# Kernel tuning notes

Hardware: AMD Instinct MI355X
Metric: run time of the kernel (lower is better)

Reference implementation:

```python
import jax, jax.numpy as jnp
import numpy as np
from jax import lax

CIN, COUT, K_EXP, KSZ = 128, 256, 8, 3
HIDDEN = CIN // 4  # reduction=4
B, H, W = 32, 56, 56
TEMP = 1.0


def setup_inputs() -> dict:
    key = jax.random.key(0)
    ks = jax.random.split(key, 6)
    x = jax.random.normal(ks[0], (B, CIN, H, W), dtype=jnp.float32)
    weight_bank = jax.random.normal(ks[1], (K_EXP, COUT, CIN, KSZ, KSZ), dtype=jnp.float32) * 0.02
    fc1_w = jax.random.normal(ks[2], (HIDDEN, CIN), dtype=jnp.float32) * (1.0 / np.sqrt(CIN))
    fc1_b = jnp.zeros((HIDDEN,), dtype=jnp.float32)
    fc2_w = jax.random.normal(ks[3], (K_EXP, HIDDEN), dtype=jnp.float32) * (1.0 / np.sqrt(HIDDEN))
    fc2_b = jnp.zeros((K_EXP,), dtype=jnp.float32)
    return {"x": x, "weight_bank": weight_bank, "fc1_w": fc1_w, "fc1_b": fc1_b,
            "fc2_w": fc2_w, "fc2_b": fc2_b}


def reference(x, weight_bank, fc1_w, fc1_b, fc2_w, fc2_b):
    b, cin, h, w = x.shape
    # Routing: GAP -> fc1 -> relu -> fc2 -> softmax(/T)
    v = jnp.mean(x, axis=(2, 3))                       # (B, cin)
    hdd = jax.nn.relu(v @ fc1_w.T + fc1_b)             # (B, hidden)
    logits = hdd @ fc2_w.T + fc2_b                     # (B, K)
    a = jax.nn.softmax(logits / TEMP, axis=1)          # (B, K)
    # Per-sample dynamic weights: (B, cout, cin, k, k)
    Wdyn = jnp.einsum('bk,kocij->bocij', a, weight_bank)
    # Batched per-sample conv via grouped convolution:
    # x -> (1, B*cin, H, W), Wdyn -> (B*cout, cin, k, k), groups=B
    xg = x.reshape(1, b * cin, h, w)
    wg = Wdyn.reshape(b * weight_bank.shape[1], cin, KSZ, KSZ)
    y = lax.conv_general_dilated(
        xg, wg,
        window_strides=(1, 1),
        padding=[(1, 1), (1, 1)],
        feature_group_count=b,
        dimension_numbers=('NCHW', 'OIHW', 'NCHW'),
    )
    return y.reshape(b, weight_bank.shape[1], y.shape[2], y.shape[3])
```

## Files before the change

kernel.cpp:

```cpp
#include <hip/hip_runtime.h>


#define CIN    128
#define COUT   256
#define KEXP   8
#define HIDDEN 32
#define B_     32
#define H_     56
#define W_     56
#define HW     3136
#define HP     58
#define WP     66
#define KK     1152

typedef float  v4f  __attribute__((ext_vector_type(4)));
typedef __bf16 v8bf __attribute__((ext_vector_type(8)));

__device__ __forceinline__ unsigned short f2bf(float x) {
  unsigned int u = __float_as_uint(x);
  u += 0x7fff + ((u >> 16) & 1);
  return (unsigned short)(u >> 16);
}
__device__ __forceinline__ float bf2f(unsigned short s) {
  return __uint_as_float(((unsigned int)s) << 16);
}

__device__ __forceinline__ void gl_lds16(const void* g, void* lds) {
  __builtin_amdgcn_global_load_lds(
      (__attribute__((address_space(1))) void*)(unsigned long long)(g),
      (__attribute__((address_space(3))) void*)(lds),
      16, 0, 0);
}

__global__ __launch_bounds__(256) void k_xpose(const float* __restrict__ x,
                                               unsigned short* __restrict__ xpt,
                                               float* __restrict__ v) {
  const int h = blockIdx.x, b = blockIdx.y, tid = threadIdx.x;
  __shared__ float tf[56 * 129];
  __shared__ float gp[256];
  const float4* xr4 = (const float4*)x + (size_t)b * CIN * 784;

#pragma unroll
  for (int it = 0; it < 7; ++it) {
    int idx = it * 256 + tid;
    int c  = idx / 14;
    int wq = idx - c * 14;
    float4 q = xr4[(size_t)c * 784 + h * 14 + wq];
    int w0 = wq * 4;
    tf[(w0 + 0) * 129 + c] = q.x;
    tf[(w0 + 1) * 129 + c] = q.y;
    tf[(w0 + 2) * 129 + c] = q.z;
    tf[(w0 + 3) * 129 + c] = q.w;
  }
  __syncthreads();

  {
    int c = tid & 127, half = tid >> 7;
    float s = 0.f;
#pragma unroll
    for (int w = half * 28; w < half * 28 + 28; ++w) s += tf[w * 129 + c];
    gp[tid] = s;
  }

#pragma unroll
  for (int it = 0; it < 7; ++it) {
    int idx = it * 256 + tid;
    int w  = idx >> 5;
    int c4 = (idx & 31) << 2;
    ushort4 o;
    o.x = f2bf(tf[w * 129 + c4 + 0]);
    o.y = f2bf(tf[w * 129 + c4 + 1]);
    o.z = f2bf(tf[w * 129 + c4 + 2]);
    o.w = f2bf(tf[w * 129 + c4 + 3]);
    *(ushort4*)(xpt + ((size_t)(b * HP + (h + 1)) * WP + (w + 1)) * CIN + c4) = o;
  }
  __syncthreads();
  if (tid < 128)
    atomicAdd(v + b * CIN + tid, (gp[tid] + gp[tid + 128]) * (1.0f / 3136.0f));
}

__global__ void k_mlp(const float* __restrict__ v, const float* __restrict__ fc1w,
                      const float* __restrict__ fc1b, const float* __restrict__ fc2w,
                      const float* __restrict__ fc2b, float* __restrict__ aout) {
  const int b = blockIdx.x, t = threadIdx.x;
  __shared__ float hid[HIDDEN];
  __shared__ float lg[KEXP];
  if (t < HIDDEN) {
    float s = fc1b[t];
    const float* vb = v + b * CIN;
    const float* wr = fc1w + t * CIN;
    for (int c = 0; c < CIN; ++c) s += vb[c] * wr[c];
    hid[t] = fmaxf(s, 0.f);
  }
  __syncthreads();
  if (t < KEXP) {
    float s = fc2b[t];
    const float* wr = fc2w + t * HIDDEN;
    for (int j = 0; j < HIDDEN; ++j) s += hid[j] * wr[j];
    lg[t] = s;
  }
  __syncthreads();
  if (t == 0) {
    float m = lg[0];
    for (int k = 1; k < KEXP; ++k) m = fmaxf(m, lg[k]);
    float e[KEXP], den = 0.f;
    for (int k = 0; k < KEXP; ++k) { e[k] = expf(lg[k] - m); den += e[k]; }
    float inv = 1.0f / den;
    for (int k = 0; k < KEXP; ++k) aout[b * KEXP + k] = e[k] * inv;
  }
}

__global__ __launch_bounds__(256) void k_wdyn(const float* __restrict__ aout,
                                              const float* __restrict__ bank,
                                              unsigned short* __restrict__ wdyn) {
  const int cout = blockIdx.x, tid = threadIdx.x;
  __shared__ float4 bS4[KEXP * 288];
  __shared__ float aS[B_ * KEXP];

#pragma unroll
  for (int k = 0; k < KEXP; ++k) {
    const float4* bp = (const float4*)(bank + (size_t)(k * COUT + cout) * KK);
    for (int it = tid; it < 288; it += 256) bS4[k * 288 + it] = bp[it];
  }
  aS[tid] = aout[tid];
  __syncthreads();

  const float* bS = (const float*)bS4;
  const int lane_kk = tid & 63;
  const int bg = tid >> 6;
  float areg[8][KEXP];
#pragma unroll
  for (int bi = 0; bi < 8; ++bi)
#pragma unroll
    for (int k = 0; k < KEXP; ++k) areg[bi][k] = aS[(bg * 8 + bi) * KEXP + k];

  for (int it = 0; it < 18; ++it) {
    int kk  = it * 64 + lane_kk;
    int khw = kk >> 7, cin = kk & 127;
    int e   = cin * 9 + khw;
    float vv[KEXP];
#pragma unroll
    for (int k = 0; k < KEXP; ++k) vv[k] = bS[k * KK + e];
#pragma unroll
    for (int bi = 0; bi < 8; ++bi) {
      float s = 0.f;
#pragma unroll
      for (int k = 0; k < KEXP; ++k) s += areg[bi][k] * vv[k];
      wdyn[(size_t)((bg * 8 + bi) * COUT + cout) * KK + kk] = f2bf(s);
    }
  }
}

__global__ __launch_bounds__(256) void k_conv(const unsigned short* __restrict__ wdyn,
                                              const unsigned short* __restrict__ xpt,
                                              float* __restrict__ out) {
  const int bx = blockIdx.x;
  const int b  = blockIdx.y;
  const int bm = bx & 1, rp = bx >> 1;
  const int h0 = rp * 2;
  const int tid = threadIdx.x;
  const int wv = tid >> 6, l = tid & 63;
  const int q = l >> 4, l15 = l & 15;
  const int mq = (wv & 1) * 64, nq = (wv >> 1) * 64;

  __shared__ __align__(16) unsigned short Ash[128 * 64];
  __shared__ __align__(16) unsigned short Bsh[128 * 64];

  const unsigned short* wb = wdyn + (size_t)(b * COUT + bm * 128) * KK;
  const unsigned short* xb = xpt + (size_t)b * HP * WP * CIN;

  v4f acc[4][4];
#pragma unroll
  for (int i = 0; i < 4; ++i)
#pragma unroll
    for (int j = 0; j < 4; ++j)
#pragma unroll
      for (int rr = 0; rr < 4; ++rr) acc[i][j][rr] = 0.f;

  for (int t = 0; t < 18; ++t) {
    const int khw = t >> 1, cinb = (t & 1) << 6;
    const int kh = khw / 3, kw = khw - 3 * kh;
#pragma unroll
    for (int it = 0; it < 4; ++it) {
      int g = it * 256 + tid;
      int row = g >> 3;
      int c = (g & 7) ^ (row & 7);
      gl_lds16(wb + (size_t)row * KK + t * 64 + c * 8,
               Ash + (it * 256 + wv * 64) * 8);
    }
#pragma unroll
    for (int it = 0; it < 4; ++it) {
      int g = it * 256 + tid;
      int p = g >> 3;
      int c = (g & 7) ^ (p & 7);
      int hh = h0 + (p >> 6) + kh;
      int ww = (p & 63) + kw;
      gl_lds16(xb + (size_t)(hh * WP + ww) * CIN + cinb + c * 8,
               Bsh + (it * 256 + wv * 64) * 8);
    }
    __syncthreads();
#pragma unroll
    for (int ks = 0; ks < 2; ++ks) {
      v8bf af[4], bfr[4];
#pragma unroll
      for (int i = 0; i < 4; ++i) {
        int row = mq + 16 * i + l15;
        int phys = (q + 4 * ks) ^ (row & 7);
        af[i] = *(const v8bf*)(Ash + (row * 8 + phys) * 8);
      }
#pragma unroll
      for (int j = 0; j < 4; ++j) {
        int p = nq + 16 * j + l15;
        int phys = (q + 4 * ks) ^ (p & 7);
        bfr[j] = *(const v8bf*)(Bsh + (p * 8 + phys) * 8);
      }
#pragma unroll
      for (int i = 0; i < 4; ++i)
#pragma unroll
        for (int j = 0; j < 4; ++j)
          acc[i][j] = __builtin_amdgcn_mfma_f32_16x16x32_bf16(af[i], bfr[j],
                                                              acc[i][j], 0, 0, 0);
    }
    __syncthreads();
  }

#pragma unroll
  for (int j = 0; j < 4; ++j) {
    int p = nq + 16 * j + l15;
    int w = p & 63, hr = h0 + (p >> 6);
    if (w < 56) {
#pragma unroll
      for (int i = 0; i < 4; ++i) {
        int cout = bm * 128 + mq + 16 * i + 4 * q;
        float* op = out + ((size_t)(b * COUT + cout) * H_ + hr) * W_ + w;
#pragma unroll
        for (int rr = 0; rr < 4; ++rr) op[(size_t)rr * HW] = acc[i][j][rr];
      }
    }
  }
}

extern "C" void kernel_launch(void* const* d_in, const int* in_sizes, int n_in,
                              void* d_out, int out_size, void* d_ws, size_t ws_size,
                              hipStream_t stream) {
  const float* x    = (const float*)d_in[0];
  const float* bank = (const float*)d_in[1];
  const float* fc1w = (const float*)d_in[2];
  const float* fc1b = (const float*)d_in[3];
  const float* fc2w = (const float*)d_in[4];
  const float* fc2b = (const float*)d_in[5];
  float* out = (float*)d_out;

  char* ws = (char*)d_ws;
  float* v    = (float*)(ws + 0);
  float* aout = (float*)(ws + 16384);
  unsigned short* wdyn = (unsigned short*)(ws + 17408);
  unsigned short* xpt  = (unsigned short*)(ws + 17408 + 18874368);

  hipMemsetAsync(v, 0, 16384, stream);
  hipMemsetAsync(xpt, 0, (size_t)B_ * HP * WP * CIN * 2, stream);

  k_xpose<<<dim3(H_, B_), 256, 0, stream>>>(x, xpt, v);
  k_mlp<<<dim3(B_), 64, 0, stream>>>(v, fc1w, fc1b, fc2w, fc2b, aout);
  k_wdyn<<<dim3(COUT), 256, 0, stream>>>(aout, bank, wdyn);
  k_conv<<<dim3(56, B_), 256, 0, stream>>>(wdyn, xpt, out);
}
```

Measured before the change: 264.1 us.

## Flatten conv pixel tiling, drop padded columns and memsets, deterministic GAP

The conv kernel now tiles over flattened 128-pixel chunks (50 tiles per image instead of 56 row-pair tiles padded to 64 columns), so no MMA work is spent on the 8 padding columns of each row. The padded input width shrinks from 66 to 58, and the halo is zeroed inside the transpose kernel, which removes the two memsets. GAP partials are written per row and summed in the MLP kernel instead of accumulated with atomics. The weight-mixing kernel moves to 512 threads with 4 samples per thread, and the last chunk clamps pixel indices, which adds some redundant loads.

Measured after the change: 250.0 us. 5.3% less time.

```diff
diff --git a/kernel.cpp b/kernel.cpp
--- a/kernel.cpp
+++ b/kernel.cpp
@@ -10,7 +10,7 @@
 #define W_     56
 #define HW     3136
 #define HP     58
-#define WP     66
+#define WP     58
 #define KK     1152
 
 typedef float  v4f  __attribute__((ext_vector_type(4)));
@@ -20,9 +20,6 @@
   unsigned int u = __float_as_uint(x);
   u += 0x7fff + ((u >> 16) & 1);
   return (unsigned short)(u >> 16);
-}
-__device__ __forceinline__ float bf2f(unsigned short s) {
-  return __uint_as_float(((unsigned int)s) << 16);
 }
 
 __device__ __forceinline__ void gl_lds16(const void* g, void* lds) {
@@ -34,7 +31,7 @@
 
 __global__ __launch_bounds__(256) void k_xpose(const float* __restrict__ x,
                                                unsigned short* __restrict__ xpt,
-                                               float* __restrict__ v) {
+                                               float* __restrict__ gpart) {
   const int h = blockIdx.x, b = blockIdx.y, tid = threadIdx.x;
   __shared__ float tf[56 * 129];
   __shared__ float gp[256];
@@ -74,22 +71,43 @@
     o.w = f2bf(tf[w * 129 + c4 + 3]);
     *(ushort4*)(xpt + ((size_t)(b * HP + (h + 1)) * WP + (w + 1)) * CIN + c4) = o;
   }
+
+  if (tid < 128) {
+    size_t rb = (size_t)(b * HP + (h + 1)) * WP * CIN;
+    xpt[rb + tid] = 0;
+    xpt[rb + 57 * CIN + tid] = 0;
+  }
+  if (h == 0 || h == 55) {
+    int hr = (h == 0) ? 0 : 57;
+    size_t rb = (size_t)(b * HP + hr) * WP * CIN;
+    ushort4 z; z.x = z.y = z.z = z.w = 0;
+    for (int i = tid; i < 1856; i += 256)
+      *(ushort4*)(xpt + rb + i * 4) = z;
+  }
+
   __syncthreads();
   if (tid < 128)
-    atomicAdd(v + b * CIN + tid, (gp[tid] + gp[tid + 128]) * (1.0f / 3136.0f));
-}
-
-__global__ void k_mlp(const float* __restrict__ v, const float* __restrict__ fc1w,
+    gpart[((size_t)h * B_ + b) * CIN + tid] =
+        (gp[tid] + gp[tid + 128]) * (1.0f / 3136.0f);
+}
+
+__global__ void k_mlp(const float* __restrict__ gpart, const float* __restrict__ fc1w,
                       const float* __restrict__ fc1b, const float* __restrict__ fc2w,
                       const float* __restrict__ fc2b, float* __restrict__ aout) {
   const int b = blockIdx.x, t = threadIdx.x;
+  __shared__ float vS[CIN];
   __shared__ float hid[HIDDEN];
   __shared__ float lg[KEXP];
+  {
+    float s = 0.f;
+    for (int h = 0; h < H_; ++h) s += gpart[((size_t)h * B_ + b) * CIN + t];
+    vS[t] = s;
+  }
+  __syncthreads();
   if (t < HIDDEN) {
     float s = fc1b[t];
-    const float* vb = v + b * CIN;
     const float* wr = fc1w + t * CIN;
-    for (int c = 0; c < CIN; ++c) s += vb[c] * wr[c];
+    for (int c = 0; c < CIN; ++c) s += vS[c] * wr[c];
     hid[t] = fmaxf(s, 0.f);
   }
   __syncthreads();
@@ -110,29 +128,28 @@
   }
 }
 
-__global__ __launch_bounds__(256) void k_wdyn(const float* __restrict__ aout,
+__global__ __launch_bounds__(512) void k_wdyn(const float* __restrict__ aout,
                                               const float* __restrict__ bank,
                                               unsigned short* __restrict__ wdyn) {
   const int cout = blockIdx.x, tid = threadIdx.x;
   __shared__ float4 bS4[KEXP * 288];
   __shared__ float aS[B_ * KEXP];
 
-#pragma unroll
-  for (int k = 0; k < KEXP; ++k) {
-    const float4* bp = (const float4*)(bank + (size_t)(k * COUT + cout) * KK);
-    for (int it = tid; it < 288; it += 256) bS4[k * 288 + it] = bp[it];
-  }
-  aS[tid] = aout[tid];
+  for (int idx = tid; idx < KEXP * 288; idx += 512) {
+    int k = idx / 288, r = idx - k * 288;
+    bS4[idx] = ((const float4*)(bank + (size_t)(k * COUT + cout) * KK))[r];
+  }
+  if (tid < 256) aS[tid] = aout[tid];
   __syncthreads();
 
   const float* bS = (const float*)bS4;
   const int lane_kk = tid & 63;
-  const int bg = tid >> 6;
-  float areg[8][KEXP];
-#pragma unroll
-  for (int bi = 0; bi < 8; ++bi)
-#pragma unroll
-    for (int k = 0; k < KEXP; ++k) areg[bi][k] = aS[(bg * 8 + bi) * KEXP + k];
+  const int sg = tid >> 6;
+  float areg[4][KEXP];
+#pragma unroll
+  for (int bi = 0; bi < 4; ++bi)
+#pragma unroll
+    for (int k = 0; k < KEXP; ++k) areg[bi][k] = aS[(sg * 4 + bi) * KEXP + k];
 
   for (int it = 0; it < 18; ++it) {
     int kk  = it * 64 + lane_kk;
@@ -142,11 +159,11 @@
 #pragma unroll
     for (int k = 0; k < KEXP; ++k) vv[k] = bS[k * KK + e];
 #pragma unroll
-    for (int bi = 0; bi < 8; ++bi) {
+    for (int bi = 0; bi < 4; ++bi) {
       float s = 0.f;
 #pragma unroll
       for (int k = 0; k < KEXP; ++k) s += areg[bi][k] * vv[k];
-      wdyn[(size_t)((bg * 8 + bi) * COUT + cout) * KK + kk] = f2bf(s);
+      wdyn[(size_t)((sg * 4 + bi) * COUT + cout) * KK + kk] = f2bf(s);
     }
   }
 }
@@ -156,8 +173,8 @@
                                               float* __restrict__ out) {
   const int bx = blockIdx.x;
   const int b  = blockIdx.y;
-  const int bm = bx & 1, rp = bx >> 1;
-  const int h0 = rp * 2;
+  const int bm = bx & 1, ch = bx >> 1;
+  const int p0 = ch * 128;
   const int tid = threadIdx.x;
   const int wv = tid >> 6, l = tid & 63;
   const int q = l >> 4, l15 = l & 15;
@@ -191,11 +208,13 @@
 #pragma unroll
     for (int it = 0; it < 4; ++it) {
       int g = it * 256 + tid;
-      int p = g >> 3;
-      int c = (g & 7) ^ (p & 7);
-      int hh = h0 + (p >> 6) + kh;
-      int ww = (p & 63) + kw;
-      gl_lds16(xb + (size_t)(hh * WP + ww) * CIN + cinb + c * 8,
+      int prow = g >> 3;
+      int c = (g & 7) ^ (prow & 7);
+      int p = p0 + prow;
+      p = p > 3135 ? 3135 : p;
+      int ph = p / 56;
+      int pw = p - ph * 56;
+      gl_lds16(xb + (size_t)((ph + kh) * WP + pw + kw) * CIN + cinb + c * 8,
                Bsh + (it * 256 + wv * 64) * 8);
     }
     __syncthreads();
@@ -226,13 +245,12 @@
 
 #pragma unroll
   for (int j = 0; j < 4; ++j) {
-    int p = nq + 16 * j + l15;
-    int w = p & 63, hr = h0 + (p >> 6);
-    if (w < 56) {
+    int p = p0 + nq + 16 * j + l15;
+    if (p < HW) {
 #pragma unroll
       for (int i = 0; i < 4; ++i) {
         int cout = bm * 128 + mq + 16 * i + 4 * q;
-        float* op = out + ((size_t)(b * COUT + cout) * H_ + hr) * W_ + w;
+        float* op = out + (size_t)(b * COUT + cout) * HW + p;
 #pragma unroll
         for (int rr = 0; rr < 4; ++rr) op[(size_t)rr * HW] = acc[i][j][rr];
       }
@@ -252,16 +270,13 @@
   float* out = (float*)d_out;
 
   char* ws = (char*)d_ws;
-  float* v    = (float*)(ws + 0);
-  float* aout = (float*)(ws + 16384);
-  unsigned short* wdyn = (unsigned short*)(ws + 17408);
-  unsigned short* xpt  = (unsigned short*)(ws + 17408 + 18874368);
-
-  hipMemsetAsync(v, 0, 16384, stream);
-  hipMemsetAsync(xpt, 0, (size_t)B_ * HP * WP * CIN * 2, stream);
-
-  k_xpose<<<dim3(H_, B_), 256, 0, stream>>>(x, xpt, v);
-  k_mlp<<<dim3(B_), 64, 0, stream>>>(v, fc1w, fc1b, fc2w, fc2b, aout);
-  k_wdyn<<<dim3(COUT), 256, 0, stream>>>(aout, bank, wdyn);
-  k_conv<<<dim3(56, B_), 256, 0, stream>>>(wdyn, xpt, out);
-}
+  float* gpart = (float*)(ws + 0);
+  float* aout  = (float*)(ws + (1u << 20));
+  unsigned short* wdyn = (unsigned short*)(ws + (2u << 20));
+  unsigned short* xpt  = (unsigned short*)(ws + (2u << 20) + 18874368);
+
+  k_xpose<<<dim3(H_, B_), 256, 0, stream>>>(x, xpt, gpart);
+  k_mlp<<<dim3(B_), 128, 0, stream>>>(gpart, fc1w, fc1b, fc2w, fc2b, aout);
+  k_wdyn<<<dim3(COUT), 512, 0, stream>>>(aout, bank, wdyn);
+  k_conv<<<dim3(50, B_), 256, 0, stream>>>(wdyn, xpt, out);
+}
```
